# Performance work log

Measured on AMD Instinct MI355X. Metric: run time of the kernel, lower is better.

Reference implementation:

```python
import jax, jax.numpy as jnp
import numpy as np

HIDDEN = 2048
NH = 16
NKV = 8
HD = 128
EPS = 1e-6
THETA = 10000.0
Q_SIZE = NH * HD
KV_SIZE = NKV * HD


def setup_inputs() -> dict:
    key = jax.random.key(0)
    k1, k2, k3, k4 = jax.random.split(key, 4)
    B, T = 2, 2048
    hidden_states = jax.random.normal(k1, (B, T, HIDDEN), dtype=jnp.float32)
    positions = jnp.broadcast_to(jnp.arange(T, dtype=jnp.int32)[None, :], (B, T))
    # learned params
    w_qkv = jax.random.normal(k2, (Q_SIZE + 2 * KV_SIZE, HIDDEN), dtype=jnp.float32) * (HIDDEN ** -0.5)
    w_o = jax.random.normal(k3, (HIDDEN, Q_SIZE), dtype=jnp.float32) * (Q_SIZE ** -0.5)
    rms_w = jnp.ones((HD,), dtype=jnp.float32) + 0.01 * jax.random.normal(k4, (HD,), dtype=jnp.float32)
    return {"positions": positions, "hidden_states": hidden_states,
            "w_qkv": w_qkv, "w_o": w_o, "rms_w": rms_w}


def _rms_norm(x, w):
    # per-head RMSNorm over last dim (head_dim)
    var = jnp.mean(jnp.square(x), axis=-1, keepdims=True)
    return x * jax.lax.rsqrt(var + EPS) * w


def _rope(positions, x):
    # NeoX-style rotary over full head_dim. positions: [B,T], x: [B,T,h,HD]
    half = HD // 2
    inv_freq = 1.0 / (THETA ** (jnp.arange(0, half, dtype=jnp.float32) / half))
    angles = positions.astype(jnp.float32)[..., None] * inv_freq  # [B,T,half]
    cos = jnp.cos(angles)[:, :, None, :]  # [B,T,1,half]
    sin = jnp.sin(angles)[:, :, None, :]
    x1, x2 = jnp.split(x, 2, axis=-1)
    return jnp.concatenate([x1 * cos - x2 * sin, x2 * cos + x1 * sin], axis=-1)


def reference(positions, hidden_states, w_qkv, w_o, rms_w):
    B, T, _ = hidden_states.shape
    qkv = jnp.einsum('bth,oh->bto', hidden_states, w_qkv)
    q = qkv[..., :Q_SIZE].reshape(B, T, NH, HD)
    k = qkv[..., Q_SIZE:Q_SIZE + KV_SIZE].reshape(B, T, NKV, HD)
    v = qkv[..., Q_SIZE + KV_SIZE:].reshape(B, T, NKV, HD)
    # QK-norm (qkv_bias=False path)
    q = _rms_norm(q, rms_w)
    k = _rms_norm(k, rms_w)
    q, k = _rope(positions, q), _rope(positions, k)
    # GQA attention, causal. group q heads onto kv heads: g = NH // NKV
    g = NH // NKV
    qg = q.reshape(B, T, NKV, g, HD)
    scale = HD ** -0.5
    scores = jnp.einsum('btkgd,bskd->bkgts', qg, k) * scale  # [B,NKV,g,T,T]
    causal = jnp.tril(jnp.ones((T, T), dtype=bool))
    scores = jnp.where(causal, scores, jnp.finfo(scores.dtype).min)
    probs = jax.nn.softmax(scores, axis=-1)
    o = jnp.einsum('bkgts,bskd->btkgd', probs, v).reshape(B, T, Q_SIZE)
    return jnp.einsum('bto,ho->bth', o, w_o)
```

## Files before the change

kernel.cpp:

```cpp
#include <hip/hip_runtime.h>
#include <hip/hip_bf16.h>

typedef __attribute__((ext_vector_type(8))) short short8;
typedef __attribute__((ext_vector_type(8))) unsigned short u16x8;
typedef __attribute__((ext_vector_type(4))) float f32x4;
typedef __attribute__((ext_vector_type(16))) float f32x16;

#define HIDDEN 2048
#define NH 16
#define NKV 8
#define HD 128
#define T_SEQ 2048
#define B_SZ 2
#define M_TOK (B_SZ * T_SEQ)
#define QSIZE (NH * HD)
#define KVSIZE (NKV * HD)
#define OUTQKV (QSIZE + 2 * KVSIZE)

__device__ __forceinline__ unsigned short f2bf(float f) {
  unsigned int u = __builtin_bit_cast(unsigned int, f);
  u += 0x7FFFu + ((u >> 16) & 1u);
  return (unsigned short)(u >> 16);
}
__device__ __forceinline__ float bf2f(unsigned short h) {
  return __builtin_bit_cast(float, (unsigned int)h << 16);
}

typedef __attribute__((address_space(3))) void lds_void;
typedef __attribute__((address_space(1))) const void glb_void;
__device__ __forceinline__ void gld16(const void* g, void* l) {
  __builtin_amdgcn_global_load_lds((glb_void*)g, (lds_void*)l, 16, 0, 0);
}

__device__ __forceinline__ float exp2fast(float x) {
  float r;
  asm("v_exp_f32 %0, %1" : "=v"(r) : "v"(x));
  return r;
}
__device__ __forceinline__ unsigned cvtpk(float lo, float hi) {
  unsigned r;
  asm("v_cvt_pk_bf16_f32 %0, %1, %2" : "=v"(r) : "v"(lo), "v"(hi));
  return r;
}
__device__ __forceinline__ void pl32swap(unsigned& a, unsigned& b) {
  asm volatile("v_permlane32_swap_b32 %0, %1" : "+v"(a), "+v"(b));
}

template <int N>
__device__ __forceinline__ void vwait();
template <> __device__ __forceinline__ void vwait<0>() { asm volatile("s_waitcnt vmcnt(0)" ::: "memory"); }
template <> __device__ __forceinline__ void vwait<3>() { asm volatile("s_waitcnt vmcnt(3)" ::: "memory"); }
template <> __device__ __forceinline__ void vwait<4>() { asm volatile("s_waitcnt vmcnt(4)" ::: "memory"); }

__device__ __forceinline__ void store4(unsigned short* p, const f32x4& v) {
  ushort4 o;
  o.x = f2bf(v[0]); o.y = f2bf(v[1]); o.z = f2bf(v[2]); o.w = f2bf(v[3]);
  *(ushort4*)p = o;
}
__device__ __forceinline__ void store4(float* p, const f32x4& v) {
  float4 o = {v[0], v[1], v[2], v[3]};
  *(float4*)p = o;
}

#define SEG0 1048576
#define SEG1 1048576
#define SEG2 524288
__global__ __launch_bounds__(256) void prep_kernel(const float* __restrict__ hidden,
                                                   const float* __restrict__ w_qkv,
                                                   const float* __restrict__ w_o,
                                                   unsigned short* __restrict__ hb,
                                                   unsigned short* __restrict__ wqkvb,
                                                   unsigned short* __restrict__ wob) {
  size_t i = (size_t)blockIdx.x * blockDim.x + threadIdx.x;
  const float* src;
  unsigned short* dst;
  if (i < SEG0) { src = hidden; dst = hb; }
  else if (i < SEG0 + SEG1) { src = w_qkv; dst = wqkvb; i -= SEG0; }
  else { src = w_o; dst = wob; i -= (SEG0 + SEG1); }
  const float4* p = (const float4*)src + i * 2;
  float4 a = p[0], b = p[1];
  u16x8 o = {f2bf(a.x), f2bf(a.y), f2bf(a.z), f2bf(a.w),
             f2bf(b.x), f2bf(b.y), f2bf(b.z), f2bf(b.w)};
  ((u16x8*)dst)[i] = o;
}

template <int MT, typename TC>
__global__ __launch_bounds__(512, 2) void gemm8(const unsigned short* __restrict__ A,
                                                const unsigned short* __restrict__ B,
                                                TC* __restrict__ C,
                                                int M, int N, int K) {
  constexpr int BM = MT * 32;
  constexpr int MT2 = MT / 2;
  constexpr int VMN = (MT == 8) ? 4 : 3;
  __shared__ unsigned short lsA[4][BM * 32];
  __shared__ unsigned short lsB[4][8192];
  const int tid = threadIdx.x;
  const int wave = tid >> 6, lane = tid & 63;
  const int wr = wave >> 2, wc = wave & 3;
  const int lr = lane & 15;
  const int ntn = N >> 8;
  const int cpx = gridDim.x >> 3;
  const int wg = (blockIdx.x & 7) * cpx + (blockIdx.x >> 3);
  const int m0 = (wg / ntn) * BM, n0 = (wg % ntn) * 256;
  const int ce = 8 * ((lane >> 4) ^ ((lr >> 1) & 3));
  const int rr0 = tid >> 2;
  const int cle = 8 * ((tid & 3) ^ ((rr0 >> 1) & 3));
  const unsigned short* pA0 = A + (size_t)(m0 + rr0) * K + cle;
  const unsigned short* pA1 = pA0 + (size_t)128 * K;
  const unsigned short* pB0 = B + (size_t)(n0 + rr0) * K + cle;
  const unsigned short* pB1 = pB0 + (size_t)128 * K;
  const int dst0 = 8 * tid, dst1 = 4096 + 8 * tid;

  auto stageA = [&](int hn) {
    const int s = hn & 3;
    gld16(pA0 + hn * 32, &lsA[s][dst0]);
    if constexpr (MT == 8) gld16(pA1 + hn * 32, &lsA[s][dst1]);
  };
  auto stageB = [&](int hn) {
    const int s = hn & 3;
    gld16(pB0 + hn * 32, &lsB[s][dst0]);
    gld16(pB1 + hn * 32, &lsB[s][dst1]);
  };

  f32x4 acc[MT][4] = {};
  short8 af[MT2], bfg[4];
  const int NT = K >> 6;

  stageA(0); stageB(0); stageA(1); stageB(1);
  vwait<0>();
  __syncthreads();

#define PHASE2(KK)                                                                        \
  {                                                                                       \
    const int slot = (sb + (KK)) & 3;                                                     \
    _Pragma("unroll")                                                                     \
    for (int j = 0; j < 4; j++)                                                           \
      bfg[j] = *(const short8*)&lsB[slot][(wc * 64 + j * 16 + lr) * 32 + ce];             \
    _Pragma("unroll")                                                                     \
    for (int i = 0; i < MT2; i++)                                                         \
      af[i] = *(const short8*)&lsA[slot][(wr * (MT * 16) + i * 16 + lr) * 32 + ce];       \
    if (st) { stageA(h2 + (KK)); stageB(h2 + (KK)); }                                     \
    if (st) vwait<VMN>(); else vwait<0>();                                                \
    __builtin_amdgcn_s_setprio(1);                                                        \
    _Pragma("unroll")                                                                     \
    for (int i = 0; i < MT2; i++)                                                         \
      _Pragma("unroll")                                                                   \
      for (int j = 0; j < 4; j++)                                                         \
        acc[i][j] =                                                                       \
            __builtin_amdgcn_mfma_f32_16x16x32_bf16(bfg[j], af[i], acc[i][j], 0, 0, 0);   \
    __builtin_amdgcn_s_setprio(0);                                                        \
    _Pragma("unroll")                                                                     \
    for (int i = 0; i < MT2; i++)                                                         \
      af[i] = *(const short8*)&lsA[slot][(wr * (MT * 16) + MT * 8 + i * 16 + lr) * 32 + ce]; \
    __builtin_amdgcn_s_setprio(1);                                                        \
    _Pragma("unroll")                                                                     \
    for (int i = 0; i < MT2; i++)                                                         \
      _Pragma("unroll")                                                                   \
      for (int j = 0; j < 4; j++)                                                         \
        acc[MT2 + i][j] =                                                                 \
            __builtin_amdgcn_mfma_f32_16x16x32_bf16(bfg[j], af[i], acc[MT2 + i][j], 0, 0, 0); \
    __builtin_amdgcn_s_setprio(0);                                                        \
    __builtin_amdgcn_s_barrier();                                                         \
  }

  for (int t = 0; t < NT; t++) {
    const int sb = (2 * t) & 3;
    const bool st = (t < NT - 1);
    const int h2 = 2 * t + 2;
    PHASE2(0)
    PHASE2(1)
  }
#undef PHASE2

#pragma unroll
  for (int i = 0; i < MT; i++)
#pragma unroll
    for (int j = 0; j < 4; j++) {
      int gm = m0 + wr * (MT * 16) + i * 16 + lr;
      int gn = n0 + wc * 64 + j * 16 + (lane >> 4) * 4;
      store4(C + (size_t)gm * N + gn, acc[i][j]);
    }
}

__global__ void norm_rope_kernel(const unsigned short* __restrict__ qkv,
                                 const int* __restrict__ positions,
                                 const float* __restrict__ rms_w,
                                 unsigned short* __restrict__ qa,
                                 unsigned short* __restrict__ ka) {
  const int m = blockIdx.x;
  const int b = m >> 11, tt = m & 2047;
  const int lane = threadIdx.x;
  const float pos = (float)positions[m];
  const float inv_freq = powf(10000.0f, -(float)lane * (1.0f / 64.0f));
  float sv, cv;
  sincosf(pos * inv_freq, &sv, &cv);
  const float w1 = rms_w[lane], w2 = rms_w[lane + 64];
  const unsigned short* src = qkv + (size_t)m * OUTQKV;
  for (int h = 0; h < 24; h++) {
    unsigned short r1 = src[h * 128 + lane], r2 = src[h * 128 + 64 + lane];
    float x1 = bf2f(r1), x2 = bf2f(r2);
    float ss = x1 * x1 + x2 * x2;
    ss += __shfl_xor(ss, 1);  ss += __shfl_xor(ss, 2);  ss += __shfl_xor(ss, 4);
    ss += __shfl_xor(ss, 8);  ss += __shfl_xor(ss, 16); ss += __shfl_xor(ss, 32);
    float rstd = rsqrtf(ss * (1.0f / 128.0f) + 1e-6f);
    float y1 = x1 * rstd * w1, y2 = x2 * rstd * w2;
    float o1 = y1 * cv - y2 * sv, o2 = y2 * cv + y1 * sv;
    unsigned short* dst;
    if (h < 16) dst = qa + (((size_t)b * NH + h) * T_SEQ + tt) * HD;
    else        dst = ka + (((size_t)b * NKV + (h - 16)) * T_SEQ + tt) * HD;
    dst[lane] = f2bf(o1); dst[lane + 64] = f2bf(o2);
  }
}

__global__ __launch_bounds__(256) void v_transpose(const unsigned short* __restrict__ qkv,
                                                   unsigned short* __restrict__ vat) {
  __shared__ unsigned short tile[64][136];
  const int tt0 = blockIdx.x * 64;
  const int kvh = blockIdx.y, b = blockIdx.z;
  const int t = threadIdx.x;
  {
    const int tok = t >> 2, d0 = (t & 3) * 32;
    const unsigned short* src = qkv + (size_t)((size_t)b * T_SEQ + tt0 + tok) * OUTQKV
                                + QSIZE + KVSIZE + kvh * HD + d0;
#pragma unroll
    for (int i = 0; i < 4; i++)
      *(u16x8*)&tile[tok][d0 + i * 8] = *(const u16x8*)(src + i * 8);
  }
  __syncthreads();
  {
    const int d = t >> 1, c0 = (t & 1) * 32;
    unsigned short* dst = vat + ((size_t)((size_t)b * NKV + kvh) * HD + d) * T_SEQ + tt0 + c0;
#pragma unroll
    for (int j = 0; j < 4; j++) {
      u16x8 v;
#pragma unroll
      for (int e = 0; e < 8; e++) v[e] = tile[c0 + j * 8 + e][d];
      *(u16x8*)(dst + j * 8) = v;
    }
  }
}

__global__ __launch_bounds__(256, 2) void attn_kernel(const unsigned short* __restrict__ qa,
                                                      const unsigned short* __restrict__ ka,
                                                      const unsigned short* __restrict__ vat,
                                                      unsigned short* __restrict__ ob) {
  __shared__ unsigned short ks[2][64 * 128];
  __shared__ unsigned short vs[2][128 * 64];
  const int bx = blockIdx.x;
  const int qt = 31 - (bx >> 4);
  const int kvh = bx & 7, b = (bx >> 3) & 1;
  const int tid = threadIdx.x, w = tid >> 6, lane = tid & 63;
  const int l31 = lane & 31, h5 = lane >> 5;
  const int h = kvh * 2 + (w >> 1);
  const int qrow = qt * 64 + (w & 1) * 32 + l31;
  const float cexp = 0.08838834764831845f * 1.44269504088896340f;

  const unsigned short* Kg = ka + ((size_t)b * NKV + kvh) * T_SEQ * HD;
  const unsigned short* Vg = vat + ((size_t)b * NKV + kvh) * (size_t)HD * T_SEQ;

  short8 qf[8];
  {
    const unsigned short* Qg = qa + (((size_t)b * NH + h) * T_SEQ + qrow) * HD;
#pragma unroll
    for (int c = 0; c < 8; c++) qf[c] = *(const short8*)(Qg + c * 16 + h5 * 8);
  }

  auto stage = [&](int j, int buf) {
#pragma unroll
    for (int s = 0; s < 4; s++) {
      int g = s * 256 + tid;
      int kr = g >> 4;
      int kc = 8 * ((g & 15) ^ (kr & 15));
      gld16(Kg + (size_t)(j * 64 + kr) * HD + kc, &ks[buf][g * 8]);
    }
#pragma unroll
    for (int s = 0; s < 4; s++) {
      int g = s * 256 + tid;
      int vd = g >> 3;
      int vc = 8 * ((g & 7) ^ (vd & 7));
      gld16(Vg + (size_t)vd * T_SEQ + j * 64 + vc, &vs[buf][g * 8]);
    }
  };

  stage(0, 0);
  vwait<0>();
  __syncthreads();

  f32x16 oacc[4] = {};
  float mraw = -1e30f, m2 = -3.0e29f, lsum = 0.f;

  for (int j = 0; j <= qt; j++) {
    const int buf = j & 1;
    if (j < qt) stage(j + 1, buf ^ 1);

    f32x16 sacc[2] = {};
    __builtin_amdgcn_s_setprio(1);
#pragma unroll
    for (int c = 0; c < 8; c++) {
#pragma unroll
      for (int t = 0; t < 2; t++) {
        const int row = t * 32 + l31;
        short8 kf = *(const short8*)&ks[buf][row * 128 + ((c * 16 + h5 * 8) ^ (8 * (l31 & 15)))];
        sacc[t] = __builtin_amdgcn_mfma_f32_32x32x16_bf16(kf, qf[c], sacc[t], 0, 0, 0);
      }
    }
    __builtin_amdgcn_s_setprio(0);

    if (j * 64 + 63 > qt * 64 + (w & 1) * 32) {
#pragma unroll
      for (int t = 0; t < 2; t++)
#pragma unroll
        for (int r = 0; r < 16; r++) {
          int kvg = j * 64 + t * 32 + (r & 3) + 8 * (r >> 2) + 4 * h5;
          if (kvg > qrow) sacc[t][r] = -1e30f;
        }
    }
    float mx = sacc[0][0];
#pragma unroll
    for (int t = 0; t < 2; t++)
#pragma unroll
      for (int r = 0; r < 16; r++) mx = fmaxf(mx, sacc[t][r]);
    mx = fmaxf(mx, __shfl_xor(mx, 32));
    if (__any((mx - mraw) * cexp > 11.5f)) {
      float mn = fmaxf(mraw, mx);
      float corr = exp2fast((mraw - mn) * cexp);
      mraw = mn;
      m2 = mn * cexp;
      lsum *= corr;
#pragma unroll
      for (int dt = 0; dt < 4; dt++)
#pragma unroll
        for (int r = 0; r < 16; r++) oacc[dt][r] *= corr;
    }
    short8 pf[4];
#pragma unroll
    for (int kt = 0; kt < 4; kt++) {
      const int t = kt >> 1, r0 = (kt & 1) * 8;
      float e0 = exp2fast(sacc[t][r0 + 0] * cexp - m2);
      float e1 = exp2fast(sacc[t][r0 + 1] * cexp - m2);
      float e2 = exp2fast(sacc[t][r0 + 2] * cexp - m2);
      float e3 = exp2fast(sacc[t][r0 + 3] * cexp - m2);
      float e4 = exp2fast(sacc[t][r0 + 4] * cexp - m2);
      float e5 = exp2fast(sacc[t][r0 + 5] * cexp - m2);
      float e6 = exp2fast(sacc[t][r0 + 6] * cexp - m2);
      float e7 = exp2fast(sacc[t][r0 + 7] * cexp - m2);
      lsum += ((e0 + e1) + (e2 + e3)) + ((e4 + e5) + (e6 + e7));
      unsigned a0 = cvtpk(e0, e1), a1 = cvtpk(e2, e3);
      unsigned b0 = cvtpk(e4, e5), b1 = cvtpk(e6, e7);
      pl32swap(a0, b0);
      pl32swap(a1, b1);
      uint4 uu = make_uint4(a0, a1, b0, b1);
      pf[kt] = __builtin_bit_cast(short8, uu);
    }
    __builtin_amdgcn_s_setprio(1);
#pragma unroll
    for (int dt = 0; dt < 4; dt++) {
      const int d = dt * 32 + l31;
#pragma unroll
      for (int kt = 0; kt < 4; kt++) {
        short8 vf = *(const short8*)&vs[buf][d * 64 + ((kt * 16 + h5 * 8) ^ (8 * (l31 & 7)))];
        oacc[dt] = __builtin_amdgcn_mfma_f32_32x32x16_bf16(vf, pf[kt], oacc[dt], 0, 0, 0);
      }
    }
    __builtin_amdgcn_s_setprio(0);
    vwait<0>();
    __syncthreads();
  }

  lsum += __shfl_xor(lsum, 32);
  const float inv = 1.0f / lsum;
  unsigned short* dst = ob + ((size_t)b * T_SEQ + qrow) * QSIZE + h * HD;
#pragma unroll
  for (int dt = 0; dt < 4; dt++)
#pragma unroll
    for (int rg = 0; rg < 4; rg++) {
      ushort4 v4;
      v4.x = f2bf(oacc[dt][rg * 4 + 0] * inv);
      v4.y = f2bf(oacc[dt][rg * 4 + 1] * inv);
      v4.z = f2bf(oacc[dt][rg * 4 + 2] * inv);
      v4.w = f2bf(oacc[dt][rg * 4 + 3] * inv);
      *(ushort4*)(dst + dt * 32 + rg * 8 + 4 * h5) = v4;
    }
}

extern "C" void kernel_launch(void* const* d_in, const int* in_sizes, int n_in,
                              void* d_out, int out_size, void* d_ws, size_t ws_size,
                              hipStream_t stream) {
  const int* positions = (const int*)d_in[0];
  const float* hidden  = (const float*)d_in[1];
  const float* w_qkv   = (const float*)d_in[2];
  const float* w_o     = (const float*)d_in[3];
  const float* rms_w   = (const float*)d_in[4];
  float* out = (float*)d_out;

  unsigned short* qkv   = (unsigned short*)d_ws;
  unsigned short* hb    = qkv + (size_t)M_TOK * OUTQKV;
  unsigned short* wqkvb = hb + (size_t)M_TOK * HIDDEN;
  unsigned short* wob   = wqkvb + (size_t)OUTQKV * HIDDEN;
  unsigned short* qa    = hb;
  unsigned short* ka    = wqkvb;
  unsigned short* vat   = wqkvb + (size_t)B_SZ * NKV * T_SEQ * HD;
  unsigned short* ob    = qkv;

  const int prep_items = SEG0 + SEG1 + SEG2;
  prep_kernel<<<prep_items / 256, 256, 0, stream>>>(hidden, w_qkv, w_o, hb, wqkvb, wob);
  gemm8<8, unsigned short>
      <<<256, 512, 0, stream>>>(hb, wqkvb, qkv, M_TOK, OUTQKV, HIDDEN);
  norm_rope_kernel<<<M_TOK, 64, 0, stream>>>(qkv, positions, rms_w, qa, ka);
  v_transpose<<<dim3(T_SEQ / 64, NKV, B_SZ), 256, 0, stream>>>(qkv, vat);
  attn_kernel<<<512, 256, 0, stream>>>(qa, ka, vat, ob);
  gemm8<4, float>
      <<<256, 512, 0, stream>>>(ob, wob, out, M_TOK, HIDDEN, QSIZE);
}
```

Before: 209.8 us.

## Replace double-buffered LDS direct loads with register-staged single buffer for occupancy

The attention kernel drops its double-buffered direct global-to-LDS staging of K/V tiles. It now prefetches the next tile into registers during compute, then writes them to a single LDS buffer after a barrier. This halves LDS use so launch bounds can ask for 3 blocks per SM instead of 2. The cost is 32 extra VGPRs for the prefetch, an extra barrier per iteration, and register pressure that may cause spills under the tighter occupancy target.

```diff
diff --git a/kernel.cpp b/kernel.cpp
--- a/kernel.cpp
+++ b/kernel.cpp
@@ -240,12 +240,12 @@
   }
 }
 
-__global__ __launch_bounds__(256, 2) void attn_kernel(const unsigned short* __restrict__ qa,
+__global__ __launch_bounds__(256, 3) void attn_kernel(const unsigned short* __restrict__ qa,
                                                       const unsigned short* __restrict__ ka,
                                                       const unsigned short* __restrict__ vat,
                                                       unsigned short* __restrict__ ob) {
-  __shared__ unsigned short ks[2][64 * 128];
-  __shared__ unsigned short vs[2][128 * 64];
+  __shared__ unsigned short ks[64 * 128];
+  __shared__ unsigned short vs[128 * 64];
   const int bx = blockIdx.x;
   const int qt = 31 - (bx >> 4);
   const int kvh = bx & 7, b = (bx >> 3) & 1;
@@ -265,33 +265,39 @@
     for (int c = 0; c < 8; c++) qf[c] = *(const short8*)(Qg + c * 16 + h5 * 8);
   }
 
-  auto stage = [&](int j, int buf) {
+  u16x8 kreg[4], vreg[4];
+  auto loadrg = [&](int j) {
 #pragma unroll
     for (int s = 0; s < 4; s++) {
       int g = s * 256 + tid;
       int kr = g >> 4;
       int kc = 8 * ((g & 15) ^ (kr & 15));
-      gld16(Kg + (size_t)(j * 64 + kr) * HD + kc, &ks[buf][g * 8]);
+      kreg[s] = *(const u16x8*)(Kg + (size_t)(j * 64 + kr) * HD + kc);
     }
 #pragma unroll
     for (int s = 0; s < 4; s++) {
       int g = s * 256 + tid;
       int vd = g >> 3;
       int vc = 8 * ((g & 7) ^ (vd & 7));
-      gld16(Vg + (size_t)vd * T_SEQ + j * 64 + vc, &vs[buf][g * 8]);
+      vreg[s] = *(const u16x8*)(Vg + (size_t)vd * T_SEQ + j * 64 + vc);
     }
   };
-
-  stage(0, 0);
-  vwait<0>();
+  auto writelds = [&]() {
+#pragma unroll
+    for (int s = 0; s < 4; s++) *(u16x8*)&ks[(s * 256 + tid) * 8] = kreg[s];
+#pragma unroll
+    for (int s = 0; s < 4; s++) *(u16x8*)&vs[(s * 256 + tid) * 8] = vreg[s];
+  };
+
+  loadrg(0);
+  writelds();
   __syncthreads();
 
   f32x16 oacc[4] = {};
   float mraw = -1e30f, m2 = -3.0e29f, lsum = 0.f;
 
   for (int j = 0; j <= qt; j++) {
-    const int buf = j & 1;
-    if (j < qt) stage(j + 1, buf ^ 1);
+    if (j < qt) loadrg(j + 1);
 
     f32x16 sacc[2] = {};
     __builtin_amdgcn_s_setprio(1);
@@ -300,7 +306,7 @@
 #pragma unroll
       for (int t = 0; t < 2; t++) {
         const int row = t * 32 + l31;
-        short8 kf = *(const short8*)&ks[buf][row * 128 + ((c * 16 + h5 * 8) ^ (8 * (l31 & 15)))];
+        short8 kf = *(const short8*)&ks[row * 128 + ((c * 16 + h5 * 8) ^ (8 * (l31 & 15)))];
         sacc[t] = __builtin_amdgcn_mfma_f32_32x32x16_bf16(kf, qf[c], sacc[t], 0, 0, 0);
       }
     }
@@ -358,13 +364,16 @@
       const int d = dt * 32 + l31;
 #pragma unroll
       for (int kt = 0; kt < 4; kt++) {
-        short8 vf = *(const short8*)&vs[buf][d * 64 + ((kt * 16 + h5 * 8) ^ (8 * (l31 & 7)))];
+        short8 vf = *(const short8*)&vs[d * 64 + ((kt * 16 + h5 * 8) ^ (8 * (l31 & 7)))];
         oacc[dt] = __builtin_amdgcn_mfma_f32_32x32x16_bf16(vf, pf[kt], oacc[dt], 0, 0, 0);
       }
     }
     __builtin_amdgcn_s_setprio(0);
-    vwait<0>();
     __syncthreads();
+    if (j < qt) {
+      writelds();
+      __syncthreads();
+    }
   }
 
   lsum += __shfl_xor(lsum, 32);
```

Result: slower. 334.8 us (+59.6%).

## Triple-buffer 32-row KV tiles in attention kernel with two-stage prefetch

Applied to the files above, without the earlier changes.

Halves the KV tile from 64 to 32 keys and replaces the double buffer with a three-slot ring, so loads run two tiles ahead and the wait at the top of each iteration allows one group of loads to stay outstanding. The aim is to hide global-to-LDS latency and drop the trailing full wait and barrier at the end of each iteration. In exchange there are twice as many iterations, each with its own barrier, max/rescale check and shuffle, and less MFMA work per barrier. The V swizzle is changed to fit the 32-wide tile.

```diff
diff --git a/kernel.cpp b/kernel.cpp
--- a/kernel.cpp
+++ b/kernel.cpp
@@ -244,8 +244,8 @@
                                                       const unsigned short* __restrict__ ka,
                                                       const unsigned short* __restrict__ vat,
                                                       unsigned short* __restrict__ ob) {
-  __shared__ unsigned short ks[2][64 * 128];
-  __shared__ unsigned short vs[2][128 * 64];
+  __shared__ unsigned short ks[3][32 * 128];
+  __shared__ unsigned short vs[3][128 * 32];
   const int bx = blockIdx.x;
   const int qt = 31 - (bx >> 4);
   const int kvh = bx & 7, b = (bx >> 3) & 1;
@@ -267,59 +267,53 @@
 
   auto stage = [&](int j, int buf) {
 #pragma unroll
-    for (int s = 0; s < 4; s++) {
+    for (int s = 0; s < 2; s++) {
       int g = s * 256 + tid;
       int kr = g >> 4;
       int kc = 8 * ((g & 15) ^ (kr & 15));
-      gld16(Kg + (size_t)(j * 64 + kr) * HD + kc, &ks[buf][g * 8]);
-    }
-#pragma unroll
-    for (int s = 0; s < 4; s++) {
+      gld16(Kg + (size_t)(j * 32 + kr) * HD + kc, &ks[buf][g * 8]);
+    }
+#pragma unroll
+    for (int s = 0; s < 2; s++) {
       int g = s * 256 + tid;
-      int vd = g >> 3;
-      int vc = 8 * ((g & 7) ^ (vd & 7));
-      gld16(Vg + (size_t)vd * T_SEQ + j * 64 + vc, &vs[buf][g * 8]);
+      int vd = g >> 2;
+      int vc = 8 * ((g & 3) ^ (vd & 3));
+      gld16(Vg + (size_t)vd * T_SEQ + j * 32 + vc, &vs[buf][g * 8]);
     }
   };
 
+  const int jmax = 2 * qt + 1;
   stage(0, 0);
-  vwait<0>();
-  __syncthreads();
+  if (jmax >= 1) stage(1, 1);
 
   f32x16 oacc[4] = {};
   float mraw = -1e30f, m2 = -3.0e29f, lsum = 0.f;
 
-  for (int j = 0; j <= qt; j++) {
-    const int buf = j & 1;
-    if (j < qt) stage(j + 1, buf ^ 1);
-
-    f32x16 sacc[2] = {};
+  for (int j = 0; j <= jmax; j++) {
+    const int buf = j % 3;
+    if (j < jmax) vwait<4>(); else vwait<0>();
+    __syncthreads();
+    if (j + 2 <= jmax) stage(j + 2, (j + 2) % 3);
+
+    f32x16 sacc = {};
     __builtin_amdgcn_s_setprio(1);
 #pragma unroll
     for (int c = 0; c < 8; c++) {
-#pragma unroll
-      for (int t = 0; t < 2; t++) {
-        const int row = t * 32 + l31;
-        short8 kf = *(const short8*)&ks[buf][row * 128 + ((c * 16 + h5 * 8) ^ (8 * (l31 & 15)))];
-        sacc[t] = __builtin_amdgcn_mfma_f32_32x32x16_bf16(kf, qf[c], sacc[t], 0, 0, 0);
+      short8 kf = *(const short8*)&ks[buf][l31 * 128 + ((c * 16 + h5 * 8) ^ (8 * (l31 & 15)))];
+      sacc = __builtin_amdgcn_mfma_f32_32x32x16_bf16(kf, qf[c], sacc, 0, 0, 0);
+    }
+    __builtin_amdgcn_s_setprio(0);
+
+    if (j * 32 + 31 > qt * 64 + (w & 1) * 32) {
+#pragma unroll
+      for (int r = 0; r < 16; r++) {
+        int kvg = j * 32 + (r & 3) + 8 * (r >> 2) + 4 * h5;
+        if (kvg > qrow) sacc[r] = -1e30f;
       }
     }
-    __builtin_amdgcn_s_setprio(0);
-
-    if (j * 64 + 63 > qt * 64 + (w & 1) * 32) {
-#pragma unroll
-      for (int t = 0; t < 2; t++)
-#pragma unroll
-        for (int r = 0; r < 16; r++) {
-          int kvg = j * 64 + t * 32 + (r & 3) + 8 * (r >> 2) + 4 * h5;
-          if (kvg > qrow) sacc[t][r] = -1e30f;
-        }
-    }
-    float mx = sacc[0][0];
-#pragma unroll
-    for (int t = 0; t < 2; t++)
-#pragma unroll
-      for (int r = 0; r < 16; r++) mx = fmaxf(mx, sacc[t][r]);
+    float mx = sacc[0];
+#pragma unroll
+    for (int r = 1; r < 16; r++) mx = fmaxf(mx, sacc[r]);
     mx = fmaxf(mx, __shfl_xor(mx, 32));
     if (__any((mx - mraw) * cexp > 11.5f)) {
       float mn = fmaxf(mraw, mx);
@@ -332,18 +326,18 @@
 #pragma unroll
         for (int r = 0; r < 16; r++) oacc[dt][r] *= corr;
     }
-    short8 pf[4];
-#pragma unroll
-    for (int kt = 0; kt < 4; kt++) {
-      const int t = kt >> 1, r0 = (kt & 1) * 8;
-      float e0 = exp2fast(sacc[t][r0 + 0] * cexp - m2);
-      float e1 = exp2fast(sacc[t][r0 + 1] * cexp - m2);
-      float e2 = exp2fast(sacc[t][r0 + 2] * cexp - m2);
-      float e3 = exp2fast(sacc[t][r0 + 3] * cexp - m2);
-      float e4 = exp2fast(sacc[t][r0 + 4] * cexp - m2);
-      float e5 = exp2fast(sacc[t][r0 + 5] * cexp - m2);
-      float e6 = exp2fast(sacc[t][r0 + 6] * cexp - m2);
-      float e7 = exp2fast(sacc[t][r0 + 7] * cexp - m2);
+    short8 pf[2];
+#pragma unroll
+    for (int kt = 0; kt < 2; kt++) {
+      const int r0 = kt * 8;
+      float e0 = exp2fast(sacc[r0 + 0] * cexp - m2);
+      float e1 = exp2fast(sacc[r0 + 1] * cexp - m2);
+      float e2 = exp2fast(sacc[r0 + 2] * cexp - m2);
+      float e3 = exp2fast(sacc[r0 + 3] * cexp - m2);
+      float e4 = exp2fast(sacc[r0 + 4] * cexp - m2);
+      float e5 = exp2fast(sacc[r0 + 5] * cexp - m2);
+      float e6 = exp2fast(sacc[r0 + 6] * cexp - m2);
+      float e7 = exp2fast(sacc[r0 + 7] * cexp - m2);
       lsum += ((e0 + e1) + (e2 + e3)) + ((e4 + e5) + (e6 + e7));
       unsigned a0 = cvtpk(e0, e1), a1 = cvtpk(e2, e3);
       unsigned b0 = cvtpk(e4, e5), b1 = cvtpk(e6, e7);
@@ -357,14 +351,12 @@
     for (int dt = 0; dt < 4; dt++) {
       const int d = dt * 32 + l31;
 #pragma unroll
-      for (int kt = 0; kt < 4; kt++) {
-        short8 vf = *(const short8*)&vs[buf][d * 64 + ((kt * 16 + h5 * 8) ^ (8 * (l31 & 7)))];
+      for (int kt = 0; kt < 2; kt++) {
+        short8 vf = *(const short8*)&vs[buf][d * 32 + 8 * ((kt * 2 + h5) ^ (d & 3))];
         oacc[dt] = __builtin_amdgcn_mfma_f32_32x32x16_bf16(vf, pf[kt], oacc[dt], 0, 0, 0);
       }
     }
     __builtin_amdgcn_s_setprio(0);
-    vwait<0>();
-    __syncthreads();
   }
 
   lsum += __shfl_xor(lsum, 32);
```

Measured after the change: 223.4 us. +6.5%, slower.

## Software-pipeline QK^T one tile ahead with triple-buffered V in attention

Applied to the files above, without the earlier changes.

The attention loop now computes the score MFMAs for the next KV tile before running softmax and PV on the current tile, so matrix work can overlap the exp and max chain. K stays double-buffered and V becomes triple-buffered, with loads issued two tiles ahead and a partial vmcnt wait (vwait<4>) at the top of each iteration. This raises LDS use from 64KB to 80KB per block and adds 32 live accumulator registers, which may reduce the two-blocks-per-CU occupancy requested by the launch bounds.

```diff
diff --git a/kernel.cpp b/kernel.cpp
--- a/kernel.cpp
+++ b/kernel.cpp
@@ -245,7 +245,7 @@
                                                       const unsigned short* __restrict__ vat,
                                                       unsigned short* __restrict__ ob) {
   __shared__ unsigned short ks[2][64 * 128];
-  __shared__ unsigned short vs[2][128 * 64];
+  __shared__ unsigned short vs[3][128 * 64];
   const int bx = blockIdx.x;
   const int qt = 31 - (bx >> 4);
   const int kvh = bx & 7, b = (bx >> 3) & 1;
@@ -265,7 +265,7 @@
     for (int c = 0; c < 8; c++) qf[c] = *(const short8*)(Qg + c * 16 + h5 * 8);
   }
 
-  auto stage = [&](int j, int buf) {
+  auto stageK = [&](int j, int buf) {
 #pragma unroll
     for (int s = 0; s < 4; s++) {
       int g = s * 256 + tid;
@@ -273,6 +273,8 @@
       int kc = 8 * ((g & 15) ^ (kr & 15));
       gld16(Kg + (size_t)(j * 64 + kr) * HD + kc, &ks[buf][g * 8]);
     }
+  };
+  auto stageV = [&](int j, int buf) {
 #pragma unroll
     for (int s = 0; s < 4; s++) {
       int g = s * 256 + tid;
@@ -282,29 +284,50 @@
     }
   };
 
-  stage(0, 0);
+  stageK(0, 0); stageV(0, 0);
+  if (qt >= 1) { stageK(1, 1); stageV(1, 1); }
   vwait<0>();
   __syncthreads();
 
+  f32x16 scur[2], snxt[2];
+  {
+    f32x16 z = {};
+    scur[0] = z; scur[1] = z;
+    __builtin_amdgcn_s_setprio(1);
+#pragma unroll
+    for (int c = 0; c < 8; c++)
+#pragma unroll
+      for (int t = 0; t < 2; t++) {
+        const int row = t * 32 + l31;
+        short8 kf = *(const short8*)&ks[0][row * 128 + ((c * 16 + h5 * 8) ^ (8 * (l31 & 15)))];
+        scur[t] = __builtin_amdgcn_mfma_f32_32x32x16_bf16(kf, qf[c], scur[t], 0, 0, 0);
+      }
+    __builtin_amdgcn_s_setprio(0);
+  }
+
   f32x16 oacc[4] = {};
   float mraw = -1e30f, m2 = -3.0e29f, lsum = 0.f;
 
   for (int j = 0; j <= qt; j++) {
-    const int buf = j & 1;
-    if (j < qt) stage(j + 1, buf ^ 1);
-
-    f32x16 sacc[2] = {};
-    __builtin_amdgcn_s_setprio(1);
-#pragma unroll
-    for (int c = 0; c < 8; c++) {
-#pragma unroll
-      for (int t = 0; t < 2; t++) {
-        const int row = t * 32 + l31;
-        short8 kf = *(const short8*)&ks[buf][row * 128 + ((c * 16 + h5 * 8) ^ (8 * (l31 & 15)))];
-        sacc[t] = __builtin_amdgcn_mfma_f32_32x32x16_bf16(kf, qf[c], sacc[t], 0, 0, 0);
-      }
-    }
-    __builtin_amdgcn_s_setprio(0);
+    if (j < qt) vwait<4>(); else vwait<0>();
+    __syncthreads();
+    if (j + 2 <= qt) { stageK(j + 2, j & 1); stageV(j + 2, (j + 2) % 3); }
+
+    if (j < qt) {
+      f32x16 z = {};
+      snxt[0] = z; snxt[1] = z;
+      const int kb = (j + 1) & 1;
+      __builtin_amdgcn_s_setprio(1);
+#pragma unroll
+      for (int c = 0; c < 8; c++)
+#pragma unroll
+        for (int t = 0; t < 2; t++) {
+          const int row = t * 32 + l31;
+          short8 kf = *(const short8*)&ks[kb][row * 128 + ((c * 16 + h5 * 8) ^ (8 * (l31 & 15)))];
+          snxt[t] = __builtin_amdgcn_mfma_f32_32x32x16_bf16(kf, qf[c], snxt[t], 0, 0, 0);
+        }
+      __builtin_amdgcn_s_setprio(0);
+    }
 
     if (j * 64 + 63 > qt * 64 + (w & 1) * 32) {
 #pragma unroll
@@ -312,14 +335,14 @@
 #pragma unroll
         for (int r = 0; r < 16; r++) {
           int kvg = j * 64 + t * 32 + (r & 3) + 8 * (r >> 2) + 4 * h5;
-          if (kvg > qrow) sacc[t][r] = -1e30f;
+          if (kvg > qrow) scur[t][r] = -1e30f;
         }
     }
-    float mx = sacc[0][0];
+    float mx = scur[0][0];
 #pragma unroll
     for (int t = 0; t < 2; t++)
 #pragma unroll
-      for (int r = 0; r < 16; r++) mx = fmaxf(mx, sacc[t][r]);
+      for (int r = 0; r < 16; r++) mx = fmaxf(mx, scur[t][r]);
     mx = fmaxf(mx, __shfl_xor(mx, 32));
     if (__any((mx - mraw) * cexp > 11.5f)) {
       float mn = fmaxf(mraw, mx);
@@ -336,14 +359,14 @@
 #pragma unroll
     for (int kt = 0; kt < 4; kt++) {
       const int t = kt >> 1, r0 = (kt & 1) * 8;
-      float e0 = exp2fast(sacc[t][r0 + 0] * cexp - m2);
-      float e1 = exp2fast(sacc[t][r0 + 1] * cexp - m2);
-      float e2 = exp2fast(sacc[t][r0 + 2] * cexp - m2);
-      float e3 = exp2fast(sacc[t][r0 + 3] * cexp - m2);
-      float e4 = exp2fast(sacc[t][r0 + 4] * cexp - m2);
-      float e5 = exp2fast(sacc[t][r0 + 5] * cexp - m2);
-      float e6 = exp2fast(sacc[t][r0 + 6] * cexp - m2);
-      float e7 = exp2fast(sacc[t][r0 + 7] * cexp - m2);
+      float e0 = exp2fast(scur[t][r0 + 0] * cexp - m2);
+      float e1 = exp2fast(scur[t][r0 + 1] * cexp - m2);
+      float e2 = exp2fast(scur[t][r0 + 2] * cexp - m2);
+      float e3 = exp2fast(scur[t][r0 + 3] * cexp - m2);
+      float e4 = exp2fast(scur[t][r0 + 4] * cexp - m2);
+      float e5 = exp2fast(scur[t][r0 + 5] * cexp - m2);
+      float e6 = exp2fast(scur[t][r0 + 6] * cexp - m2);
+      float e7 = exp2fast(scur[t][r0 + 7] * cexp - m2);
       lsum += ((e0 + e1) + (e2 + e3)) + ((e4 + e5) + (e6 + e7));
       unsigned a0 = cvtpk(e0, e1), a1 = cvtpk(e2, e3);
       unsigned b0 = cvtpk(e4, e5), b1 = cvtpk(e6, e7);
@@ -352,19 +375,20 @@
       uint4 uu = make_uint4(a0, a1, b0, b1);
       pf[kt] = __builtin_bit_cast(short8, uu);
     }
+    const int vb = j % 3;
     __builtin_amdgcn_s_setprio(1);
 #pragma unroll
     for (int dt = 0; dt < 4; dt++) {
       const int d = dt * 32 + l31;
 #pragma unroll
       for (int kt = 0; kt < 4; kt++) {
-        short8 vf = *(const short8*)&vs[buf][d * 64 + ((kt * 16 + h5 * 8) ^ (8 * (l31 & 7)))];
+        short8 vf = *(const short8*)&vs[vb][d * 64 + ((kt * 16 + h5 * 8) ^ (8 * (l31 & 7)))];
         oacc[dt] = __builtin_amdgcn_mfma_f32_32x32x16_bf16(vf, pf[kt], oacc[dt], 0, 0, 0);
       }
     }
     __builtin_amdgcn_s_setprio(0);
-    vwait<0>();
-    __syncthreads();
+    scur[0] = snxt[0];
+    scur[1] = snxt[1];
   }
 
   lsum += __shfl_xor(lsum, 32);
```

After: 210.5 us. About the same (+0.3%).
